# Performance work log

Measured on AMD Instinct MI355X. Metric: run time of the kernel, lower is better.

The kernel has to match this reference:

```python
import jax, jax.numpy as jnp
import numpy as np

B = 8192
D_IN = 10
H = 1900


def _l2norm_cols(w):
    # tf.nn.l2_normalize(w, dim=0): normalize each column, eps 1e-12
    sq = jnp.sum(w * w, axis=0, keepdims=True)
    return w * jax.lax.rsqrt(jnp.maximum(sq, 1e-12))


def setup_inputs() -> dict:
    key = jax.random.key(0)
    ks = jax.random.split(key, 12)
    return {
        "inputs": jax.random.normal(ks[0], (B, D_IN), jnp.float32),
        "c_prev": jax.random.normal(ks[1], (B, H), jnp.float32),
        "h_prev": jax.random.normal(ks[2], (B, H), jnp.float32),
        "wx": jax.random.normal(ks[3], (D_IN, 4 * H), jnp.float32) * 0.1,
        "wh": jax.random.normal(ks[4], (H, 4 * H), jnp.float32) * 0.1,
        "wmx": jax.random.normal(ks[5], (D_IN, H), jnp.float32) * 0.1,
        "wmh": jax.random.normal(ks[6], (H, H), jnp.float32) * 0.1,
        "b": jax.random.normal(ks[7], (4 * H,), jnp.float32) * 0.1,
        "gx": jax.random.uniform(ks[8], (4 * H,), jnp.float32, 0.5, 1.5),
        "gh": jax.random.uniform(ks[9], (4 * H,), jnp.float32, 0.5, 1.5),
        "gmx": jax.random.uniform(ks[10], (H,), jnp.float32, 0.5, 1.5),
        "gmh": jax.random.uniform(ks[11], (H,), jnp.float32, 0.5, 1.5),
    }


def reference(inputs, c_prev, h_prev, wx, wh, wmx, wmh, b, gx, gh, gmx, gmh):
    # weight-normalized weights (per-column l2 norm * gain)
    wx_n = _l2norm_cols(wx) * gx
    wh_n = _l2norm_cols(wh) * gh
    wmx_n = _l2norm_cols(wmx) * gmx
    wmh_n = _l2norm_cols(wmh) * gmh
    # multiplicative state m: [B, H]
    m = (inputs @ wmx_n) * (h_prev @ wmh_n)
    # gate pre-activations z: [B, 4H]
    z = inputs @ wx_n + m @ wh_n + b
    i, f, o, u = jnp.split(z, 4, axis=1)
    i = jax.nn.sigmoid(i)
    f = jax.nn.sigmoid(f)
    o = jax.nn.sigmoid(o)
    u = jnp.tanh(u)
    c = f * c_prev + i * u
    h = o * jnp.tanh(c)
    return (h, c)
```

## Files before the change

kernel.cpp:

```cpp
#include <hip/hip_runtime.h>

typedef unsigned short ushort_t;
typedef short bf16x8 __attribute__((ext_vector_type(8)));
typedef float f32x4 __attribute__((ext_vector_type(4)));

#define H 1900
#define FH 7600
#define BATCH 8192
#define KP 1952
#define NP_A 1920
#define NB 7680
#define BK 32
#define KITERS (KP / BK)

#define NKT 30

static const size_t OFF_SWX  = 0;
static const size_t OFF_SWH  = 32768;
static const size_t OFF_SWMX = 65536;
static const size_t OFF_SWMH = 73728;
static const size_t OFF_WMXN = 81920;
static const size_t OFF_PART = 163840;
static const size_t OFF_HBF  = 786432;
static const size_t OFF_MEXT = OFF_HBF + 31981568;
static const size_t OFF_WMHT = OFF_MEXT + 31981568;
static const size_t OFF_WHXT = OFF_WMHT + 7495680;

#define PW_X  0
#define PW_H  60800
#define PW_MX 121600
#define PW_MH 136800

#define BAR() __builtin_amdgcn_s_barrier()
#define PRIO1 __builtin_amdgcn_s_setprio(1)
#define PRIO0 __builtin_amdgcn_s_setprio(0)
#define WAIT_LGKM0 asm volatile("s_waitcnt lgkmcnt(0)" ::: "memory")
#define WAIT_VM(N) asm volatile("s_waitcnt vmcnt(" #N ")" ::: "memory")

__device__ __forceinline__ ushort_t f2bf(float x) {
  unsigned u = __float_as_uint(x);
  return (ushort_t)((u + 0x7fffu + ((u >> 16) & 1u)) >> 16);
}

__device__ __forceinline__ void gl_lds16(const ushort_t* g, ushort_t* lds) {
  __builtin_amdgcn_global_load_lds(
      (const __attribute__((address_space(1))) unsigned int*)(g),
      (__attribute__((address_space(3))) unsigned int*)(lds), 16, 0, 0);
}

__global__ void colsum_partial_kernel(const float* __restrict__ wx, const float* __restrict__ wh,
                                      const float* __restrict__ wmx, const float* __restrict__ wmh,
                                      float* __restrict__ parts) {
  int c = blockIdx.x * 256 + threadIdx.x;
  int y = blockIdx.y, p = blockIdx.z;
  const float* W; int K, N; float* out;
  if (y == 0)      { W = wx;  K = 10;   N = FH; out = parts + PW_X  + (size_t)p * FH; }
  else if (y == 1) { W = wh;  K = 1900; N = FH; out = parts + PW_H  + (size_t)p * FH; }
  else if (y == 2) { W = wmx; K = 10;   N = H;  out = parts + PW_MX + (size_t)p * H;  }
  else             { W = wmh; K = 1900; N = H;  out = parts + PW_MH + (size_t)p * H;  }
  if (c >= N) return;
  int rp = (K + 7) / 8;
  int r0 = p * rp, r1 = r0 + rp; if (r1 > K) r1 = K;
  float s = 0.f;
  for (int r = r0; r < r1; ++r) { float v = W[(size_t)r * N + c]; s += v * v; }
  out[c] = s;
}

__global__ void scales_final_kernel(const float* __restrict__ parts,
                                    const float* __restrict__ gx, const float* __restrict__ gh,
                                    const float* __restrict__ gmx, const float* __restrict__ gmh,
                                    float* __restrict__ s_wx, float* __restrict__ s_wh,
                                    float* __restrict__ s_wmx, float* __restrict__ s_wmh) {
  int c = blockIdx.x * 256 + threadIdx.x;
  int y = blockIdx.y;
  const float* pp; int N; const float* g; float* out;
  if (y == 0)      { pp = parts + PW_X;  N = FH; g = gx;  out = s_wx;  }
  else if (y == 1) { pp = parts + PW_H;  N = FH; g = gh;  out = s_wh;  }
  else if (y == 2) { pp = parts + PW_MX; N = H;  g = gmx; out = s_wmx; }
  else             { pp = parts + PW_MH; N = H;  g = gmh; out = s_wmh; }
  if (c >= N) return;
  float s = 0.f;
  for (int p = 0; p < 8; ++p) s += pp[(size_t)p * N + c];
  out[c] = g[c] * rsqrtf(fmaxf(s, 1e-12f));
}

__global__ void cvt_h_kernel(const float* __restrict__ h_prev, ushort_t* __restrict__ hbf) {
  size_t idx = (size_t)blockIdx.x * 256 + threadIdx.x;
  int row = (int)(idx / KP), col = (int)(idx % KP);
  float v = (col < H) ? h_prev[(size_t)row * H + col] : 0.f;
  hbf[idx] = f2bf(v);
}

__global__ void wmxn_kernel(const float* __restrict__ wmx, const float* __restrict__ s_wmx,
                            float* __restrict__ wmxn) {
  int idx = blockIdx.x * 256 + threadIdx.x;
  int i = idx / NP_A, j = idx - i * NP_A;
  wmxn[idx] = (j < H) ? wmx[i * H + j] * s_wmx[j] : 0.f;
}

__global__ void wmhT_kernel(const float* __restrict__ wmh, const float* __restrict__ s_wmh,
                            ushort_t* __restrict__ wmhT) {
  __shared__ float tile[32][33];
  int n0 = blockIdx.x * 32, k0 = blockIdx.y * 32;
  int tx = threadIdx.x & 31, ty = threadIdx.x >> 5;
#pragma unroll
  for (int it = 0; it < 4; ++it) {
    int k = k0 + ty + it * 8, n = n0 + tx;
    float v = (k < H && n < H) ? wmh[(size_t)k * H + n] : 0.f;
    tile[ty + it * 8][tx] = v;
  }
  __syncthreads();
#pragma unroll
  for (int it = 0; it < 4; ++it) {
    int n = n0 + ty + it * 8, k = k0 + tx;
    float v = tile[tx][ty + it * 8];
    float s = (n < H) ? s_wmh[n] : 0.f;
    wmhT[(size_t)n * KP + k] = f2bf(v * s);
  }
}

__global__ void whxT_kernel(const float* __restrict__ wh, const float* __restrict__ wx,
                            const float* __restrict__ s_wh, const float* __restrict__ s_wx,
                            ushort_t* __restrict__ whxT) {
  __shared__ float tile[32][33];
  int c0 = blockIdx.x * 32, k0 = blockIdx.y * 32;
  int tx = threadIdx.x & 31, ty = threadIdx.x >> 5;
#pragma unroll
  for (int it = 0; it < 4; ++it) {
    int k = k0 + ty + it * 8, c = c0 + tx;
    float v = 0.f;
    if (c < FH) {
      if (k < H) v = wh[(size_t)k * FH + c] * s_wh[c];
      else if (k >= NP_A && k < NP_A + 10) v = wx[(size_t)(k - NP_A) * FH + c] * s_wx[c];
    }
    tile[ty + it * 8][tx] = v;
  }
  __syncthreads();
#pragma unroll
  for (int it = 0; it < 4; ++it) {
    int c = c0 + ty + it * 8, k = k0 + tx;
    if (c < FH) {
      int g = c / H; int j = c - g * H; int n = 4 * j + g;
      whxT[(size_t)n * KP + k] = f2bf(tile[tx][ty + it * 8]);
    }
  }
}

__global__ void mext_tail_kernel(const float* __restrict__ inputs, ushort_t* __restrict__ m_ext) {
  int idx = blockIdx.x * 256 + threadIdx.x;
  int row = idx >> 5, c = idx & 31;
  float v = (c < 10) ? inputs[(size_t)row * 10 + c] : 0.f;
  m_ext[(size_t)row * KP + NP_A + c] = f2bf(v);
}

__global__ void whxT_tail_kernel(ushort_t* __restrict__ whxT) {
  int idx = blockIdx.x * 256 + threadIdx.x;
  whxT[(size_t)FH * KP + idx] = 0;
}

__device__ __forceinline__ void gemm_tile128(const ushort_t* __restrict__ Ag,
                                             const ushort_t* __restrict__ Bg,
                                             int m0, int n0,
                                             ushort_t* As, ushort_t* Bs,
                                             f32x4 acc[4][4]) {
  const int tid = threadIdx.x;
  const int lane = tid & 63;
  const int quad = lane >> 4;
  const int lo = lane & 15;
  const int wave = tid >> 6;
  const int wm = (wave & 1) << 6;
  const int wn = (wave >> 1) << 6;
  const int sw = (lo >> 1) & 3;

  const int cr = lane >> 2;
  const int hg = (lane & 3) ^ ((lane >> 3) & 3);
  const int r0 = wave * 16 + cr;
  const int r1 = 64 + wave * 16 + cr;
  const ushort_t* gA0 = Ag + (size_t)(m0 + r0) * KP + hg * 8;
  const ushort_t* gA1 = Ag + (size_t)(m0 + r1) * KP + hg * 8;
  const ushort_t* gB0 = Bg + (size_t)(n0 + r0) * KP + hg * 8;
  const ushort_t* gB1 = Bg + (size_t)(n0 + r1) * KP + hg * 8;
  ushort_t* lA0 = As + (wave * 16) * BK;
  ushort_t* lA1 = As + (64 + wave * 16) * BK;
  ushort_t* lB0 = Bs + (wave * 16) * BK;
  ushort_t* lB1 = Bs + (64 + wave * 16) * BK;

  for (int kt = 0; kt < KITERS; ++kt) {
    __syncthreads();
    gl_lds16(gA0, lA0);
    gl_lds16(gA1, lA1);
    gl_lds16(gB0, lB0);
    gl_lds16(gB1, lB1);
    __syncthreads();
    bf16x8 af[4], bfv[4];
#pragma unroll
    for (int mf = 0; mf < 4; ++mf)
      af[mf] = *(const bf16x8*)(As + (wm + mf * 16 + lo) * BK + ((quad ^ sw) << 3));
#pragma unroll
    for (int nf = 0; nf < 4; ++nf)
      bfv[nf] = *(const bf16x8*)(Bs + (wn + nf * 16 + lo) * BK + ((quad ^ sw) << 3));
#pragma unroll
    for (int mf = 0; mf < 4; ++mf)
#pragma unroll
      for (int nf = 0; nf < 4; ++nf)
        acc[mf][nf] = __builtin_amdgcn_mfma_f32_16x16x32_bf16(af[mf], bfv[nf], acc[mf][nf], 0, 0, 0);
    gA0 += BK; gA1 += BK; gB0 += BK; gB1 += BK;
  }
}

__global__ void __launch_bounds__(256) gemmA_kernel(const ushort_t* __restrict__ hbf,
                                                    const ushort_t* __restrict__ wmhT,
                                                    const float* __restrict__ inputs,
                                                    const float* __restrict__ wmxn,
                                                    ushort_t* __restrict__ m_ext) {
  __shared__ __align__(16) char smem[16384];
  ushort_t* As = (ushort_t*)smem;
  ushort_t* Bs = (ushort_t*)(smem + 8192);
  f32x4 acc[4][4];
  f32x4 zv = {0.f, 0.f, 0.f, 0.f};
#pragma unroll
  for (int a = 0; a < 4; ++a)
#pragma unroll
    for (int bq = 0; bq < 4; ++bq) acc[a][bq] = zv;
  int m0 = blockIdx.x * 128, n0 = blockIdx.y * 128;
  gemm_tile128(hbf, wmhT, m0, n0, As, Bs, acc);
  __syncthreads();
  float* inL  = (float*)smem;
  float* wmxL = (float*)(smem + 5120);
  for (int t = threadIdx.x; t < 1280; t += 256) {
    int r = t / 10, i = t - r * 10;
    inL[t] = inputs[(size_t)(m0 + r) * 10 + i];
  }
  for (int t = threadIdx.x; t < 1280; t += 256) {
    int i = t >> 7, c = t & 127;
    wmxL[t] = wmxn[i * NP_A + n0 + c];
  }
  __syncthreads();
  const int lane = threadIdx.x & 63, quad = lane >> 4, lo = lane & 15;
  const int wave = threadIdx.x >> 6, wm = (wave & 1) << 6, wn = (wave >> 1) << 6;
#pragma unroll
  for (int mf = 0; mf < 4; ++mf)
#pragma unroll
    for (int r = 0; r < 4; ++r) {
      int rl = wm + mf * 16 + quad * 4 + r;
      float inrow[10];
#pragma unroll
      for (int i = 0; i < 10; ++i) inrow[i] = inL[rl * 10 + i];
#pragma unroll
      for (int nf = 0; nf < 4; ++nf) {
        int cl = wn + nf * 16 + lo;
        float mx = 0.f;
#pragma unroll
        for (int i = 0; i < 10; ++i) mx += inrow[i] * wmxL[i * 128 + cl];
        float mv = acc[mf][nf][r] * mx;
        m_ext[(size_t)(m0 + rl) * KP + (n0 + cl)] = f2bf(mv);
      }
    }
}


__device__ __forceinline__ void stage_half(const ushort_t* __restrict__ G, int Rg, int kb,
                                           ushort_t* L, int tid) {
  const int wave = tid >> 6;
#pragma unroll
  for (int q = 0; q < 2; ++q) {
    const int idx = q * 512 + tid;
    const int r = idx >> 3, s = idx & 7;
    const int gs = s ^ (r & 7);
    gl_lds16(G + (size_t)(Rg + r) * KP + kb + gs * 8,
             L + (size_t)(q * 512 + wave * 64) * 8);
  }
}

__device__ __forceinline__ void read_Ahalf(const ushort_t* A, int wmL, int lo, int mh,
                                           int sw0, int sw1, bf16x8 af[8]) {
#pragma unroll
  for (int mf = 0; mf < 4; ++mf) {
    const ushort_t* p = A + ((wmL + mh * 64 + mf * 16 + lo) << 6);
    af[mf * 2 + 0] = *(const bf16x8*)(p + sw0);
    af[mf * 2 + 1] = *(const bf16x8*)(p + sw1);
  }
}

__device__ __forceinline__ void read_Bhalf(const ushort_t* B, int wnL, int lo, int nh,
                                           int sw0, int sw1, bf16x8 bf[4]) {
#pragma unroll
  for (int nf = 0; nf < 2; ++nf) {
    const ushort_t* p = B + ((wnL + nh * 32 + nf * 16 + lo) << 6);
    bf[nf * 2 + 0] = *(const bf16x8*)(p + sw0);
    bf[nf * 2 + 1] = *(const bf16x8*)(p + sw1);
  }
}

__device__ __forceinline__ void mfma_quad(const bf16x8 af[8], const bf16x8 bf[4],
                                          f32x4 acc[8][4], int mh, int nh) {
#pragma unroll
  for (int mf = 0; mf < 4; ++mf)
#pragma unroll
    for (int nf = 0; nf < 2; ++nf) {
      f32x4 c = acc[mh * 4 + mf][nh * 2 + nf];
      c = __builtin_amdgcn_mfma_f32_16x16x32_bf16(af[mf * 2 + 0], bf[nf * 2 + 0], c, 0, 0, 0);
      c = __builtin_amdgcn_mfma_f32_16x16x32_bf16(af[mf * 2 + 1], bf[nf * 2 + 1], c, 0, 0, 0);
      acc[mh * 4 + mf][nh * 2 + nf] = c;
    }
}

template <int MODE>
__device__ __forceinline__ void b8_iter(const ushort_t* __restrict__ Ag,
                                        const ushort_t* __restrict__ Bg,
                                        int m0, int n0, int T,
                                        ushort_t* Acur, ushort_t* Bcur,
                                        ushort_t* Anxt, ushort_t* Bnxt,
                                        int tid, int lo, int wmL, int wnL,
                                        int sw0, int sw1, f32x4 acc[8][4]) {
  bf16x8 af[8], b0f[4], b1f[4];
  read_Ahalf(Acur, wmL, lo, 0, sw0, sw1, af);
  read_Bhalf(Bcur, wnL, lo, 0, sw0, sw1, b0f);
  if (MODE <= 1) stage_half(Ag, m0 + 128, (T + 1) * 64, Anxt + 8192, tid);
  BAR(); WAIT_LGKM0;
  PRIO1; mfma_quad(af, b0f, acc, 0, 0); PRIO0;
  BAR();
  read_Bhalf(Bcur, wnL, lo, 1, sw0, sw1, b1f);
  BAR(); WAIT_LGKM0;
  PRIO1; mfma_quad(af, b1f, acc, 0, 1); PRIO0;
  BAR();
  read_Ahalf(Acur, wmL, lo, 1, sw0, sw1, af);
  if (MODE == 0) stage_half(Bg, n0, (T + 2) * 64, Bcur, tid);
  BAR(); WAIT_LGKM0;
  PRIO1; mfma_quad(af, b1f, acc, 1, 1); PRIO0;
  BAR();
  if (MODE == 0) {
    stage_half(Ag, m0, (T + 2) * 64, Acur, tid);
    stage_half(Bg, n0 + 128, (T + 2) * 64, Bcur + 8192, tid);
    WAIT_VM(6);
  } else if (MODE == 1) {
    WAIT_VM(0);
  }
  BAR();
  PRIO1; mfma_quad(af, b0f, acc, 1, 0); PRIO0;
  BAR();
}

__global__ void __launch_bounds__(512, 2)
gemmB8_kernel(const ushort_t* __restrict__ mext, const ushort_t* __restrict__ whxT,
              const float* __restrict__ bvec, const float* __restrict__ c_prev,
              float* __restrict__ hout, float* __restrict__ cout) {
  extern __shared__ __align__(16) char smem[];
  ushort_t* As0 = (ushort_t*)smem;
  ushort_t* Bs0 = (ushort_t*)(smem + 32768);
  ushort_t* As1 = (ushort_t*)(smem + 65536);
  ushort_t* Bs1 = (ushort_t*)(smem + 98304);

  const int tid = threadIdx.x;
  const int lane = tid & 63;
  const int lo = lane & 15, quad = lane >> 4;
  const int wave = tid >> 6;
  const int wmL = (wave & 1) << 7;
  const int wnL = (wave >> 1) << 6;
  const int sw0 = ((quad ^ (lo & 7)) << 3);
  const int sw1 = (((4 | quad) ^ (lo & 7)) << 3);

  int bid = blockIdx.x;
  int swz = (bid & 7) * 120 + (bid >> 3);
  int mt = swz & 31, nt = swz >> 5;
  int m0 = mt << 8, n0 = nt << 8;

  f32x4 acc[8][4];
  f32x4 zv = {0.f, 0.f, 0.f, 0.f};
#pragma unroll
  for (int a = 0; a < 8; ++a)
#pragma unroll
    for (int bq = 0; bq < 4; ++bq) acc[a][bq] = zv;

  const ushort_t* Ag = mext;
  const ushort_t* Bg = whxT;

  stage_half(Ag, m0,       0,  As0,        tid);
  stage_half(Bg, n0,       0,  Bs0,        tid);
  stage_half(Ag, m0 + 128, 0,  As0 + 8192, tid);
  stage_half(Bg, n0 + 128, 0,  Bs0 + 8192, tid);
  stage_half(Bg, n0,       64, Bs1,        tid);
  stage_half(Ag, m0,       64, As1,        tid);
  stage_half(Bg, n0 + 128, 64, Bs1 + 8192, tid);
  WAIT_VM(6);
  BAR();

  for (int T = 0; T < NKT - 2; T += 2) {
    b8_iter<0>(Ag, Bg, m0, n0, T,     As0, Bs0, As1, Bs1, tid, lo, wmL, wnL, sw0, sw1, acc);
    b8_iter<0>(Ag, Bg, m0, n0, T + 1, As1, Bs1, As0, Bs0, tid, lo, wmL, wnL, sw0, sw1, acc);
  }
  b8_iter<1>(Ag, Bg, m0, n0, NKT - 2, As0, Bs0, As1, Bs1, tid, lo, wmL, wnL, sw0, sw1, acc);
  b8_iter<2>(Ag, Bg, m0, n0, NKT - 1, As1, Bs1, As0, Bs0, tid, lo, wmL, wnL, sw0, sw1, acc);

  {
    const int wavei = tid >> 6;
#pragma unroll
    for (int q = 0; q < 2; ++q) {
      const int idx = q * 512 + tid;
      const int r = idx >> 2, s = idx & 3;
      const int gs = s ^ (r & 3);
      gl_lds16(Ag + (size_t)(m0 + r) * KP + 1920 + gs * 8,
               As0 + (size_t)(q * 512 + wavei * 64) * 8);
    }
#pragma unroll
    for (int q = 0; q < 2; ++q) {
      const int idx = q * 512 + tid;
      const int r = idx >> 2, s = idx & 3;
      const int gs = s ^ (r & 3);
      gl_lds16(Bg + (size_t)(n0 + r) * KP + 1920 + gs * 8,
               Bs0 + (size_t)(q * 512 + wavei * 64) * 8);
    }
    WAIT_VM(0);
    BAR();
    const int swt = ((quad ^ (lo & 3)) << 3);
    bf16x8 a2[8], b2[4];
#pragma unroll
    for (int mf = 0; mf < 8; ++mf)
      a2[mf] = *(const bf16x8*)(As0 + ((wmL + mf * 16 + lo) << 5) + swt);
#pragma unroll
    for (int nf = 0; nf < 4; ++nf)
      b2[nf] = *(const bf16x8*)(Bs0 + ((wnL + nf * 16 + lo) << 5) + swt);
#pragma unroll
    for (int mf = 0; mf < 8; ++mf)
#pragma unroll
      for (int nf = 0; nf < 4; ++nf)
        acc[mf][nf] = __builtin_amdgcn_mfma_f32_16x16x32_bf16(a2[mf], b2[nf], acc[mf][nf], 0, 0, 0);
  }

#pragma unroll
  for (int nf = 0; nf < 4; ++nf) {
    int gn = n0 + wnL + nf * 16 + lo;
    int j = gn >> 2, g = gn & 3;
    float bias = (j < H) ? bvec[g * H + j] : 0.f;
#pragma unroll
    for (int mf = 0; mf < 8; ++mf)
#pragma unroll
      for (int r = 0; r < 4; ++r) {
        float zs = acc[mf][nf][r] + bias;
        float v1 = __shfl_xor(zs, 1);
        float v2 = __shfl_xor(zs, 2);
        float v3 = __shfl_xor(v1, 2);
        if (g == r && j < H) {
          float zi, zf, zo, zu;
          { int t = 0 ^ g; zi = t == 0 ? zs : t == 1 ? v1 : t == 2 ? v2 : v3; }
          { int t = 1 ^ g; zf = t == 0 ? zs : t == 1 ? v1 : t == 2 ? v2 : v3; }
          { int t = 2 ^ g; zo = t == 0 ? zs : t == 1 ? v1 : t == 2 ? v2 : v3; }
          { int t = 3 ^ g; zu = t == 0 ? zs : t == 1 ? v1 : t == 2 ? v2 : v3; }
          float iv = 1.f / (1.f + __expf(-zi));
          float fv = 1.f / (1.f + __expf(-zf));
          float ov = 1.f / (1.f + __expf(-zo));
          float uv = tanhf(zu);
          int row = m0 + wmL + mf * 16 + quad * 4 + r;
          size_t oidx = (size_t)row * H + j;
          float cp = c_prev[oidx];
          float cv = fv * cp + iv * uv;
          hout[oidx] = ov * tanhf(cv);
          cout[oidx] = cv;
        }
      }
  }
}

extern "C" void kernel_launch(void* const* d_in, const int* in_sizes, int n_in,
                              void* d_out, int out_size, void* d_ws, size_t ws_size,
                              hipStream_t stream) {
  const float* inputs = (const float*)d_in[0];
  const float* c_prev = (const float*)d_in[1];
  const float* h_prev = (const float*)d_in[2];
  const float* wx  = (const float*)d_in[3];
  const float* wh  = (const float*)d_in[4];
  const float* wmx = (const float*)d_in[5];
  const float* wmh = (const float*)d_in[6];
  const float* bv  = (const float*)d_in[7];
  const float* gx  = (const float*)d_in[8];
  const float* gh  = (const float*)d_in[9];
  const float* gmx = (const float*)d_in[10];
  const float* gmh = (const float*)d_in[11];

  char* ws = (char*)d_ws;
  float* s_wx  = (float*)(ws + OFF_SWX);
  float* s_wh  = (float*)(ws + OFF_SWH);
  float* s_wmx = (float*)(ws + OFF_SWMX);
  float* s_wmh = (float*)(ws + OFF_SWMH);
  float* wmxn  = (float*)(ws + OFF_WMXN);
  float* parts = (float*)(ws + OFF_PART);
  ushort_t* hbf   = (ushort_t*)(ws + OFF_HBF);
  ushort_t* m_ext = (ushort_t*)(ws + OFF_MEXT);
  ushort_t* wmhT  = (ushort_t*)(ws + OFF_WMHT);
  ushort_t* whxT  = (ushort_t*)(ws + OFF_WHXT);

  float* hout = (float*)d_out;
  float* cout = hout + (size_t)BATCH * H;

  static bool attr_set = false;
  if (!attr_set) {
    hipFuncSetAttribute(reinterpret_cast<const void*>(&gemmB8_kernel),
                        hipFuncAttributeMaxDynamicSharedMemorySize, 131072);
    attr_set = true;
  }

  colsum_partial_kernel<<<dim3(30, 4, 8), 256, 0, stream>>>(wx, wh, wmx, wmh, parts);
  scales_final_kernel<<<dim3(30, 4), 256, 0, stream>>>(parts, gx, gh, gmx, gmh,
                                                       s_wx, s_wh, s_wmx, s_wmh);
  cvt_h_kernel<<<62464, 256, 0, stream>>>(h_prev, hbf);
  wmxn_kernel<<<75, 256, 0, stream>>>(wmx, s_wmx, wmxn);
  wmhT_kernel<<<dim3(60, 61), 256, 0, stream>>>(wmh, s_wmh, wmhT);
  whxT_kernel<<<dim3(238, 61), 256, 0, stream>>>(wh, wx, s_wh, s_wx, whxT);
  mext_tail_kernel<<<1024, 256, 0, stream>>>(inputs, m_ext);
  whxT_tail_kernel<<<610, 256, 0, stream>>>(whxT);
  gemmA_kernel<<<dim3(64, 15), 256, 0, stream>>>(hbf, wmhT, inputs, wmxn, m_ext);
  gemmB8_kernel<<<dim3(960), 512, 131072, stream>>>(m_ext, whxT, bv, c_prev, hout, cout);
}
```

Measured before the change: 1.093 ms.

## Store GEMM operands in 256-row k-tiled panels and remap block-to-XCD tiles

The bf16 operands m_ext and whxT move from row-major (row*KP) storage to a panel-tiled layout. Each 256-row panel holds contiguous 256x64 k-tiles followed by a 32-wide tail, so every staged 16 KB chunk is one contiguous global region. The block-index mapping is also changed so each XCD gets a compact group of 8 M-tiles by 15 N-tiles, with the aim of better L2 reuse. In exchange the producer kernels must write with scattered tiled addresses, and the tail-zeroing kernel now uses div/mod indexing.

Result: faster. 1.052 ms (-3.8%).

```diff
diff --git a/kernel.cpp b/kernel.cpp
--- a/kernel.cpp
+++ b/kernel.cpp
@@ -14,6 +14,9 @@
 #define KITERS (KP / BK)
 
 #define NKT 30
+#define KT_U 16384
+#define TAIL_U 491520
+#define PANEL_U 499712
 
 static const size_t OFF_SWX  = 0;
 static const size_t OFF_SWH  = 32768;
@@ -46,6 +49,14 @@
   __builtin_amdgcn_global_load_lds(
       (const __attribute__((address_space(1))) unsigned int*)(g),
       (__attribute__((address_space(3))) unsigned int*)(lds), 16, 0, 0);
+}
+
+__device__ __forceinline__ size_t tiled_addr(int row, int col) {
+  return (size_t)(row >> 8) * PANEL_U + (size_t)(col >> 6) * KT_U +
+         (size_t)(row & 255) * 64 + (col & 63);
+}
+__device__ __forceinline__ size_t tiled_addr_tail(int row, int ctail) {
+  return (size_t)(row >> 8) * PANEL_U + TAIL_U + (size_t)(row & 255) * 32 + ctail;
 }
 
 __global__ void colsum_partial_kernel(const float* __restrict__ wx, const float* __restrict__ wh,
@@ -141,7 +152,8 @@
     int c = c0 + ty + it * 8, k = k0 + tx;
     if (c < FH) {
       int g = c / H; int j = c - g * H; int n = 4 * j + g;
-      whxT[(size_t)n * KP + k] = f2bf(tile[tx][ty + it * 8]);
+      size_t a = (k < NP_A) ? tiled_addr(n, k) : tiled_addr_tail(n, k - NP_A);
+      whxT[a] = f2bf(tile[tx][ty + it * 8]);
     }
   }
 }
@@ -150,12 +162,14 @@
   int idx = blockIdx.x * 256 + threadIdx.x;
   int row = idx >> 5, c = idx & 31;
   float v = (c < 10) ? inputs[(size_t)row * 10 + c] : 0.f;
-  m_ext[(size_t)row * KP + NP_A + c] = f2bf(v);
+  m_ext[tiled_addr_tail(row, c)] = f2bf(v);
 }
 
 __global__ void whxT_tail_kernel(ushort_t* __restrict__ whxT) {
   int idx = blockIdx.x * 256 + threadIdx.x;
-  whxT[(size_t)FH * KP + idx] = 0;
+  int n = 7600 + idx / 1952, k = idx % 1952;
+  size_t a = (k < NP_A) ? tiled_addr(n, k) : tiled_addr_tail(n, k - NP_A);
+  whxT[a] = 0;
 }
 
 __device__ __forceinline__ void gemm_tile128(const ushort_t* __restrict__ Ag,
@@ -253,13 +267,13 @@
 #pragma unroll
         for (int i = 0; i < 10; ++i) mx += inrow[i] * wmxL[i * 128 + cl];
         float mv = acc[mf][nf][r] * mx;
-        m_ext[(size_t)(m0 + rl) * KP + (n0 + cl)] = f2bf(mv);
+        m_ext[tiled_addr(m0 + rl, n0 + cl)] = f2bf(mv);
       }
     }
 }
 
 
-__device__ __forceinline__ void stage_half(const ushort_t* __restrict__ G, int Rg, int kb,
+__device__ __forceinline__ void stage_half(const ushort_t* __restrict__ Gp, int rbase, int kt,
                                            ushort_t* L, int tid) {
   const int wave = tid >> 6;
 #pragma unroll
@@ -267,7 +281,7 @@
     const int idx = q * 512 + tid;
     const int r = idx >> 3, s = idx & 7;
     const int gs = s ^ (r & 7);
-    gl_lds16(G + (size_t)(Rg + r) * KP + kb + gs * 8,
+    gl_lds16(Gp + (size_t)kt * KT_U + (size_t)(rbase + r) * 64 + gs * 8,
              L + (size_t)(q * 512 + wave * 64) * 8);
   }
 }
@@ -306,9 +320,9 @@
 }
 
 template <int MODE>
-__device__ __forceinline__ void b8_iter(const ushort_t* __restrict__ Ag,
-                                        const ushort_t* __restrict__ Bg,
-                                        int m0, int n0, int T,
+__device__ __forceinline__ void b8_iter(const ushort_t* __restrict__ Ap,
+                                        const ushort_t* __restrict__ Bp,
+                                        int T,
                                         ushort_t* Acur, ushort_t* Bcur,
                                         ushort_t* Anxt, ushort_t* Bnxt,
                                         int tid, int lo, int wmL, int wnL,
@@ -316,7 +330,7 @@
   bf16x8 af[8], b0f[4], b1f[4];
   read_Ahalf(Acur, wmL, lo, 0, sw0, sw1, af);
   read_Bhalf(Bcur, wnL, lo, 0, sw0, sw1, b0f);
-  if (MODE <= 1) stage_half(Ag, m0 + 128, (T + 1) * 64, Anxt + 8192, tid);
+  if (MODE <= 1) stage_half(Ap, 128, T + 1, Anxt + 8192, tid);
   BAR(); WAIT_LGKM0;
   PRIO1; mfma_quad(af, b0f, acc, 0, 0); PRIO0;
   BAR();
@@ -325,13 +339,13 @@
   PRIO1; mfma_quad(af, b1f, acc, 0, 1); PRIO0;
   BAR();
   read_Ahalf(Acur, wmL, lo, 1, sw0, sw1, af);
-  if (MODE == 0) stage_half(Bg, n0, (T + 2) * 64, Bcur, tid);
+  if (MODE == 0) stage_half(Bp, 0, T + 2, Bcur, tid);
   BAR(); WAIT_LGKM0;
   PRIO1; mfma_quad(af, b1f, acc, 1, 1); PRIO0;
   BAR();
   if (MODE == 0) {
-    stage_half(Ag, m0, (T + 2) * 64, Acur, tid);
-    stage_half(Bg, n0 + 128, (T + 2) * 64, Bcur + 8192, tid);
+    stage_half(Ap, 0, T + 2, Acur, tid);
+    stage_half(Bp, 128, T + 2, Bcur + 8192, tid);
     WAIT_VM(6);
   } else if (MODE == 1) {
     WAIT_VM(0);
@@ -361,8 +375,9 @@
   const int sw1 = (((4 | quad) ^ (lo & 7)) << 3);
 
   int bid = blockIdx.x;
-  int swz = (bid & 7) * 120 + (bid >> 3);
-  int mt = swz & 31, nt = swz >> 5;
+  int xcd = bid & 7, j = bid >> 3;
+  int mt = ((xcd & 3) << 3) | (j & 7);
+  int nt = (xcd >> 2) * 15 + (j >> 3);
   int m0 = mt << 8, n0 = nt << 8;
 
   f32x4 acc[8][4];
@@ -372,25 +387,25 @@
 #pragma unroll
     for (int bq = 0; bq < 4; ++bq) acc[a][bq] = zv;
 
-  const ushort_t* Ag = mext;
-  const ushort_t* Bg = whxT;
-
-  stage_half(Ag, m0,       0,  As0,        tid);
-  stage_half(Bg, n0,       0,  Bs0,        tid);
-  stage_half(Ag, m0 + 128, 0,  As0 + 8192, tid);
-  stage_half(Bg, n0 + 128, 0,  Bs0 + 8192, tid);
-  stage_half(Bg, n0,       64, Bs1,        tid);
-  stage_half(Ag, m0,       64, As1,        tid);
-  stage_half(Bg, n0 + 128, 64, Bs1 + 8192, tid);
+  const ushort_t* Ap = mext + (size_t)mt * PANEL_U;
+  const ushort_t* Bp = whxT + (size_t)nt * PANEL_U;
+
+  stage_half(Ap, 0,   0, As0,        tid);
+  stage_half(Bp, 0,   0, Bs0,        tid);
+  stage_half(Ap, 128, 0, As0 + 8192, tid);
+  stage_half(Bp, 128, 0, Bs0 + 8192, tid);
+  stage_half(Bp, 0,   1, Bs1,        tid);
+  stage_half(Ap, 0,   1, As1,        tid);
+  stage_half(Bp, 128, 1, Bs1 + 8192, tid);
   WAIT_VM(6);
   BAR();
 
   for (int T = 0; T < NKT - 2; T += 2) {
-    b8_iter<0>(Ag, Bg, m0, n0, T,     As0, Bs0, As1, Bs1, tid, lo, wmL, wnL, sw0, sw1, acc);
-    b8_iter<0>(Ag, Bg, m0, n0, T + 1, As1, Bs1, As0, Bs0, tid, lo, wmL, wnL, sw0, sw1, acc);
-  }
-  b8_iter<1>(Ag, Bg, m0, n0, NKT - 2, As0, Bs0, As1, Bs1, tid, lo, wmL, wnL, sw0, sw1, acc);
-  b8_iter<2>(Ag, Bg, m0, n0, NKT - 1, As1, Bs1, As0, Bs0, tid, lo, wmL, wnL, sw0, sw1, acc);
+    b8_iter<0>(Ap, Bp, T,     As0, Bs0, As1, Bs1, tid, lo, wmL, wnL, sw0, sw1, acc);
+    b8_iter<0>(Ap, Bp, T + 1, As1, Bs1, As0, Bs0, tid, lo, wmL, wnL, sw0, sw1, acc);
+  }
+  b8_iter<1>(Ap, Bp, NKT - 2, As0, Bs0, As1, Bs1, tid, lo, wmL, wnL, sw0, sw1, acc);
+  b8_iter<2>(Ap, Bp, NKT - 1, As1, Bs1, As0, Bs0, tid, lo, wmL, wnL, sw0, sw1, acc);
 
   {
     const int wavei = tid >> 6;
@@ -399,7 +414,7 @@
       const int idx = q * 512 + tid;
       const int r = idx >> 2, s = idx & 3;
       const int gs = s ^ (r & 3);
-      gl_lds16(Ag + (size_t)(m0 + r) * KP + 1920 + gs * 8,
+      gl_lds16(Ap + TAIL_U + (size_t)r * 32 + gs * 8,
                As0 + (size_t)(q * 512 + wavei * 64) * 8);
     }
 #pragma unroll
@@ -407,7 +422,7 @@
       const int idx = q * 512 + tid;
       const int r = idx >> 2, s = idx & 3;
       const int gs = s ^ (r & 3);
-      gl_lds16(Bg + (size_t)(n0 + r) * KP + 1920 + gs * 8,
+      gl_lds16(Bp + TAIL_U + (size_t)r * 32 + gs * 8,
                Bs0 + (size_t)(q * 512 + wavei * 64) * 8);
     }
     WAIT_VM(0);
@@ -430,8 +445,8 @@
 #pragma unroll
   for (int nf = 0; nf < 4; ++nf) {
     int gn = n0 + wnL + nf * 16 + lo;
-    int j = gn >> 2, g = gn & 3;
-    float bias = (j < H) ? bvec[g * H + j] : 0.f;
+    int j2 = gn >> 2, g = gn & 3;
+    float bias = (j2 < H) ? bvec[g * H + j2] : 0.f;
 #pragma unroll
     for (int mf = 0; mf < 8; ++mf)
 #pragma unroll
@@ -440,7 +455,7 @@
         float v1 = __shfl_xor(zs, 1);
         float v2 = __shfl_xor(zs, 2);
         float v3 = __shfl_xor(v1, 2);
-        if (g == r && j < H) {
+        if (g == r && j2 < H) {
           float zi, zf, zo, zu;
           { int t = 0 ^ g; zi = t == 0 ? zs : t == 1 ? v1 : t == 2 ? v2 : v3; }
           { int t = 1 ^ g; zf = t == 0 ? zs : t == 1 ? v1 : t == 2 ? v2 : v3; }
@@ -451,7 +466,7 @@
           float ov = 1.f / (1.f + __expf(-zo));
           float uv = tanhf(zu);
           int row = m0 + wmL + mf * 16 + quad * 4 + r;
-          size_t oidx = (size_t)row * H + j;
+          size_t oidx = (size_t)row * H + j2;
           float cp = c_prev[oidx];
           float cv = fv * cp + iv * uv;
           hout[oidx] = ov * tanhf(cv);
```
